# Optimization experiments

Hardware: AMD Instinct MI355X
Metric: run time of the kernel (lower is better)

The kernel has to match this reference:

```python
import jax, jax.numpy as jnp
import numpy as np

D_MODEL = 2048
NHEADS = 16
ROPE_DIM = 64      # config.rope['head_dim']
NOPE_DIM = 128     # config.nope_head_dim
V_DIM = 128        # config.v_head_dim
Q_LORA = 1536      # config.q_lora_rank
KV_LORA = 512      # config.kv_lora_rank
ROPE_BASE = 10000.0
EPS = 1e-6
Q_HEAD = NOPE_DIM + ROPE_DIM   # 192
KV_HEAD = NOPE_DIM + V_DIM     # 256


def rms_norm(x, w):
    return x * jax.lax.rsqrt(jnp.mean(x * x, axis=-1, keepdims=True) + EPS) * w


def apply_rope(x, offset=0):
    # x: (B, H, T, d); standard rotate-half RoPE, positions offset by past length
    d, t = x.shape[-1], x.shape[2]
    inv_freq = 1.0 / (ROPE_BASE ** (jnp.arange(0, d, 2, dtype=jnp.float32) / d))
    pos = jnp.arange(offset, offset + t, dtype=jnp.float32)
    f = pos[:, None] * inv_freq[None, :]          # (T, d/2)
    cos = jnp.concatenate([jnp.cos(f), jnp.cos(f)], -1).astype(x.dtype)
    sin = jnp.concatenate([jnp.sin(f), jnp.sin(f)], -1).astype(x.dtype)
    x1, x2 = jnp.split(x, 2, axis=-1)
    rot = jnp.concatenate([-x2, x1], -1)
    return x * cos + rot * sin


def setup_inputs() -> dict:
    key = jax.random.key(0)
    ks = jax.random.split(key, 8)
    s = 0.02
    return {
        'x': jax.random.normal(ks[0], (2, 2048, D_MODEL), jnp.float32),
        'q_a_w': jax.random.normal(ks[1], (D_MODEL, Q_LORA), jnp.float32) * s,
        'q_a_norm_w': jnp.ones((Q_LORA,), jnp.float32),
        'q_b_w': jax.random.normal(ks[2], (Q_LORA, NHEADS * Q_HEAD), jnp.float32) * s,
        'kv_a_w': jax.random.normal(ks[3], (D_MODEL, KV_LORA + ROPE_DIM), jnp.float32) * s,
        'kv_norm_w': jnp.ones((KV_LORA,), jnp.float32),
        'kv_b_w': jax.random.normal(ks[4], (KV_LORA, NHEADS * KV_HEAD), jnp.float32) * s,
        'o_w': jax.random.normal(ks[5], (NHEADS * V_DIM, D_MODEL), jnp.float32) * s,
    }


def reference(x, q_a_w, q_a_norm_w, q_b_w, kv_a_w, kv_norm_w, kv_b_w, o_w):
    B, T, _ = x.shape
    # Query: LoRA down-proj -> RMSNorm -> up-proj
    q = rms_norm(x @ q_a_w, q_a_norm_w) @ q_b_w            # (B,T,H*Q_HEAD)
    q = q.reshape(B, T, NHEADS, Q_HEAD).transpose(0, 2, 1, 3)
    q_nope, q_rope = q[..., :NOPE_DIM], q[..., NOPE_DIM:]
    # KV: joint compressed projection, split into latent + shared rope key
    kv = x @ kv_a_w                                         # (B,T,KV_LORA+ROPE_DIM)
    kv_c, k_rope = kv[..., :KV_LORA], kv[..., KV_LORA:]
    k_rope = k_rope[:, None, :, :]                          # (B,1,T,ROPE_DIM) - MQA rope key
    kvb = rms_norm(kv_c, kv_norm_w) @ kv_b_w                # (B,T,H*KV_HEAD)
    kvb = kvb.reshape(B, T, NHEADS, KV_HEAD).transpose(0, 2, 1, 3)
    k_nope, v = kvb[..., :NOPE_DIM], kvb[..., NOPE_DIM:]
    # Decoupled RoPE (prefill: offset 0)
    q_rope = apply_rope(q_rope)
    k_rope = apply_rope(k_rope)
    qs = jnp.concatenate([q_nope, q_rope], -1)              # (B,H,T,Q_HEAD)
    ks = jnp.concatenate([k_nope, jnp.broadcast_to(k_rope, (B, NHEADS, T, ROPE_DIM))], -1)
    # SDPA with causal mask, scale = 1/sqrt(q_head_dim)
    scale = 1.0 / np.sqrt(Q_HEAD).astype(np.float32)
    scores = jnp.einsum('bhqd,bhkd->bhqk', qs, ks) * scale
    mask = jnp.tril(jnp.ones((T, T), bool))
    scores = jnp.where(mask[None, None], scores, jnp.finfo(scores.dtype).min)
    attn = jax.nn.softmax(scores, axis=-1)
    out = jnp.einsum('bhqk,bhkd->bhqd', attn, v)            # (B,H,T,V_DIM)
    out = out.transpose(0, 2, 1, 3).reshape(B, T, NHEADS * V_DIM)
    return out @ o_w                                        # (B,T,d_model)
```

## Files before the change

### kernel.cpp

```cpp
#include <hip/hip_runtime.h>
#include <hip/hip_bf16.h>
#include <math.h>

#define NHEADS 16
#define SEQ 2048
#define BATCH 2
#define NTOK (BATCH * SEQ)
#define EPSF 1e-6f

typedef short bf16x8 __attribute__((ext_vector_type(8)));
typedef float f32x4 __attribute__((ext_vector_type(4)));

__device__ __forceinline__ unsigned short f2bf(float v) {
    __hip_bfloat16 h = __float2bfloat16(v);
    return *reinterpret_cast<unsigned short*>(&h);
}
__device__ __forceinline__ float bf2f(unsigned short u) {
    __hip_bfloat16 h = *reinterpret_cast<__hip_bfloat16*>(&u);
    return __bfloat162float(h);
}
__device__ __forceinline__ void g2l16(const void* g, void* l) {
    __builtin_amdgcn_global_load_lds(
        (const __attribute__((address_space(1))) void*)g,
        (__attribute__((address_space(3))) void*)l, 16, 0, 0);
}

#define ROPE_L2 0.4152410118609203f

__global__ __launch_bounds__(256) void cvt_bf16(
    const float* __restrict__ in, unsigned short* __restrict__ out)
{
    const int i = blockIdx.x * 256 + threadIdx.x;
    float4 a = ((const float4*)in)[i * 2];
    float4 b = ((const float4*)in)[i * 2 + 1];
    unsigned short o[8] = {f2bf(a.x), f2bf(a.y), f2bf(a.z), f2bf(a.w),
                           f2bf(b.x), f2bf(b.y), f2bf(b.z), f2bf(b.w)};
    *(bf16x8*)(out + (size_t)i * 8) = *(bf16x8*)o;
}

struct WSeg { const float* src; unsigned short* dst; int Nw, K, nx, off; };
struct WSegs { WSeg s[5]; };

__global__ __launch_bounds__(256) void prep_weights(WSegs segs)
{
    __shared__ float T[32][33];
    const int bid = blockIdx.x;
    int si = 0;
#pragma unroll
    for (int i = 1; i < 5; ++i) si += (bid >= segs.s[i].off) ? 1 : 0;
    const WSeg sg = segs.s[si];
    const int local = bid - sg.off;
    const int bx = local % sg.nx, by = local / sg.nx;
    const int n0 = bx * 32, k0 = by * 32;
    const int tid = threadIdx.x;
    const int r = tid >> 3, c4 = (tid & 7) * 4;
    const bool valid = (n0 < sg.Nw);
    if (valid) {
        float4 v = *(const float4*)(sg.src + (size_t)(k0 + r) * sg.Nw + n0 + c4);
        T[r][c4 + 0] = v.x; T[r][c4 + 1] = v.y; T[r][c4 + 2] = v.z; T[r][c4 + 3] = v.w;
    }
    __syncthreads();
    unsigned short o[4];
#pragma unroll
    for (int j = 0; j < 4; ++j) o[j] = valid ? f2bf(T[c4 + j][r]) : (unsigned short)0;
    *(ulong1*)(sg.dst + (size_t)(n0 + r) * sg.K + k0 + c4) = *(ulong1*)o;
}

template <int OUT_BF16>
__global__ __launch_bounds__(256) void gemm_bt(
    const unsigned short* __restrict__ A,
    const unsigned short* __restrict__ Bt,
    void* __restrict__ Cv,
    int K, int N)
{
    __shared__ __align__(16) unsigned short As[128 * 32];
    __shared__ __align__(16) unsigned short Bs[128 * 32];
    const int tid = threadIdx.x;
    const int lane = tid & 63, wid = tid >> 6;
    const int l16 = lane & 15, lq = lane >> 4;
    const int wr = wid >> 1, wc = wid & 1;
    const int bm = blockIdx.y * 128, bn = blockIdx.x * 128;

    f32x4 acc[4][4];
#pragma unroll
    for (int m = 0; m < 4; ++m)
#pragma unroll
        for (int n = 0; n < 4; ++n) acc[m][n] = (f32x4){0.f, 0.f, 0.f, 0.f};

    for (int k0 = 0; k0 < K; k0 += 32) {
        __syncthreads();
#pragma unroll
        for (int t = 0; t < 2; ++t) {
            const int chunk = t * 256 + tid;
            const int row = chunk >> 2, koff = (chunk & 3) << 3;
            g2l16(A  + (size_t)(bm + row) * K + k0 + koff, (char*)As + chunk * 16);
            g2l16(Bt + (size_t)(bn + row) * K + k0 + koff, (char*)Bs + chunk * 16);
        }
        __syncthreads();

        bf16x8 af[4], bfr[4];
#pragma unroll
        for (int m = 0; m < 4; ++m)
            af[m] = *(const bf16x8*)(As + (wr * 64 + m * 16 + l16) * 32 + lq * 8);
#pragma unroll
        for (int n = 0; n < 4; ++n)
            bfr[n] = *(const bf16x8*)(Bs + (wc * 64 + n * 16 + l16) * 32 + lq * 8);
#pragma unroll
        for (int m = 0; m < 4; ++m)
#pragma unroll
            for (int n = 0; n < 4; ++n)
                acc[m][n] = __builtin_amdgcn_mfma_f32_16x16x32_bf16(af[m], bfr[n], acc[m][n], 0, 0, 0);
    }

#pragma unroll
    for (int m = 0; m < 4; ++m)
#pragma unroll
        for (int n = 0; n < 4; ++n)
#pragma unroll
            for (int reg = 0; reg < 4; ++reg) {
                const int row = bm + wr * 64 + m * 16 + lq * 4 + reg;
                const int col = bn + wc * 64 + n * 16 + l16;
                if (OUT_BF16) ((unsigned short*)Cv)[(size_t)row * N + col] = f2bf(acc[m][n][reg]);
                else          ((float*)Cv)[(size_t)row * N + col] = acc[m][n][reg];
            }
}

__global__ __launch_bounds__(256) void rmsnorm_bf(
    const float* __restrict__ in, const float* __restrict__ w,
    unsigned short* __restrict__ out, int in_stride, int cols)
{
    const int row = blockIdx.x;
    const float* p = in + (size_t)row * in_stride;
    float ss = 0.f;
    for (int c = threadIdx.x; c < cols; c += 256) { float v = p[c]; ss += v * v; }
#pragma unroll
    for (int off = 32; off > 0; off >>= 1) ss += __shfl_down(ss, off, 64);
    __shared__ float wsum[4];
    __shared__ float s_scale;
    const int wave = threadIdx.x >> 6;
    if ((threadIdx.x & 63) == 0) wsum[wave] = ss;
    __syncthreads();
    if (threadIdx.x == 0) {
        float t = wsum[0] + wsum[1] + wsum[2] + wsum[3];
        s_scale = rsqrtf(t / (float)cols + EPSF);
    }
    __syncthreads();
    const float sc = s_scale;
    for (int c = threadIdx.x; c < cols; c += 256)
        out[(size_t)row * cols + c] = f2bf(p[c] * sc * w[c]);
}

__global__ __launch_bounds__(256) void rmsnorm_kv_rope(
    const float* __restrict__ in, const float* __restrict__ w,
    unsigned short* __restrict__ kv_out, unsigned short* __restrict__ krope_out)
{
    const int row = blockIdx.x;
    const float* p = in + (size_t)row * 2176;
    const int tid = threadIdx.x;
    float v0 = p[tid], v1 = p[tid + 256];
    float ss = v0 * v0 + v1 * v1;
#pragma unroll
    for (int off = 32; off > 0; off >>= 1) ss += __shfl_down(ss, off, 64);
    __shared__ float wsum[4];
    __shared__ float s_scale;
    const int wave = tid >> 6;
    if ((tid & 63) == 0) wsum[wave] = ss;
    __syncthreads();
    if (tid == 0) {
        float t = wsum[0] + wsum[1] + wsum[2] + wsum[3];
        s_scale = rsqrtf(t / 512.0f + EPSF);
    }
    __syncthreads();
    const float sc = s_scale;
    kv_out[(size_t)row * 512 + tid]       = f2bf(v0 * sc * w[tid]);
    kv_out[(size_t)row * 512 + tid + 256] = f2bf(v1 * sc * w[tid + 256]);
    if (tid < 64) {
        const int s = row & (SEQ - 1);
        const int j = tid, jj = j & 31;
        float inv = exp2f(-ROPE_L2 * (float)jj);
        float f = (float)s * inv;
        float sn, cs;
        sincosf(f, &sn, &cs);
        const float* kb = p + 512;
        float v = (j < 32) ? (kb[j] * cs - kb[j + 32] * sn)
                           : (kb[j] * cs + kb[j - 32] * sn);
        krope_out[(size_t)row * 64 + j] = f2bf(v);
    }
}

__global__ __launch_bounds__(256) void pack_vt(
    const unsigned short* __restrict__ kvb, unsigned short* __restrict__ vt_bf)
{
    __shared__ __align__(16) unsigned short T[64][136];
    const int st = blockIdx.x, h = blockIdx.y, b = blockIdx.z;
    const int tid = threadIdx.x;
#pragma unroll
    for (int t = 0; t < 4; ++t) {
        int i = tid + t * 256;
        int r = i >> 4, c8 = i & 15;
        bf16x8 v = *(const bf16x8*)(kvb + (size_t)(b * SEQ + st * 64 + r) * 4096 + h * 256 + 128 + c8 * 8);
        *(bf16x8*)&T[r][c8 * 8] = v;
    }
    __syncthreads();
    const int d = tid >> 1, sh = (tid & 1) * 32;
    unsigned short tmp[32];
#pragma unroll
    for (int k = 0; k < 32; ++k) tmp[k] = T[sh + k][d];
    unsigned short* dst = vt_bf + ((size_t)(b * NHEADS + h) * 128 + d) * SEQ + st * 64 + sh;
#pragma unroll
    for (int c = 0; c < 4; ++c) *(bf16x8*)(dst + c * 8) = *(bf16x8*)&tmp[c * 8];
}

#define KPD 200
#define VPD 72
#define PPD 72

__global__ __launch_bounds__(256) void flash_mfma(
    const unsigned short* __restrict__ qbuf,
    const unsigned short* __restrict__ kvb,
    const unsigned short* __restrict__ krope,
    const unsigned short* __restrict__ vt,
    unsigned short* __restrict__ ctx)
{
    __shared__ __align__(16) unsigned short Ks[64][KPD];
    __shared__ __align__(16) unsigned short Vs[128][VPD];
    __shared__ __align__(16) unsigned short Ps[4][16][PPD];
    const int id = blockIdx.x;
    const int xcd = id & 7, sl = id >> 3;
    const int grp = sl >> 4, pair = sl & 15;
    const int hb = xcd + 8 * grp;
    const int h = hb & 15, b = hb >> 4;
    const int tid = threadIdx.x;
    const int wid = tid >> 6, lane = tid & 63;
    const int l16 = lane & 15, lq = lane >> 4;

    const size_t headV = (size_t)(b * NHEADS + h) * 128 * SEQ;
    const float scale = 0.07216878364870323f;

    float cs8[8], sn8[8];
    const int vrow = tid >> 1, vg = tid & 1;

    bf16x8 kn[4], kr[2], vv[4];

#define FLASH_LOAD(KT)                                                          \
    {                                                                           \
        const int tk0_ = b * SEQ + (KT) * 64;                                   \
        _Pragma("unroll")                                                       \
        for (int t = 0; t < 4; ++t) {                                           \
            int i_ = tid + t * 256, r_ = i_ >> 4, c8_ = i_ & 15;                \
            kn[t] = *(const bf16x8*)(kvb + (size_t)(tk0_ + r_) * 4096 + h * 256 + c8_ * 8); \
        }                                                                       \
        _Pragma("unroll")                                                       \
        for (int t = 0; t < 2; ++t) {                                           \
            int i_ = tid + t * 256, r_ = i_ >> 3, c8_ = i_ & 7;                 \
            kr[t] = *(const bf16x8*)(krope + (size_t)(tk0_ + r_) * 64 + c8_ * 8); \
        }                                                                       \
        const unsigned short* vsrc_ = vt + headV + (size_t)vrow * SEQ + (KT) * 64 + vg * 8; \
        _Pragma("unroll")                                                       \
        for (int j = 0; j < 4; ++j) vv[j] = *(const bf16x8*)(vsrc_ + j * 16);   \
    }

#pragma unroll
    for (int pass = 0; pass < 2; ++pass) {
        const int qt = pass ? (31 - pair) : pair;
        const int srow = qt * 64 + wid * 16 + l16;

        bf16x8 qf[6];
        {
            const unsigned short* qp = qbuf + (size_t)(b * SEQ + srow) * 3072 + h * 192 + lq * 8;
            bf16x8 raw[6];
#pragma unroll
            for (int kk = 0; kk < 6; ++kk) raw[kk] = *(const bf16x8*)(qp + kk * 32);
#pragma unroll
            for (int jj = 0; jj < 8; ++jj) {
                float inv = exp2f(-ROPE_L2 * (float)(lq * 8 + jj));
                sincosf((float)srow * inv, &sn8[jj], &cs8[jj]);
            }
#pragma unroll
            for (int kk = 0; kk < 4; ++kk) {
                unsigned short o[8];
#pragma unroll
                for (int e = 0; e < 8; ++e) o[e] = f2bf(bf2f(((unsigned short*)&raw[kk])[e]) * scale);
                qf[kk] = *(bf16x8*)o;
            }
            unsigned short o4[8], o5[8];
#pragma unroll
            for (int e = 0; e < 8; ++e) {
                float x1 = bf2f(((unsigned short*)&raw[4])[e]);
                float x2 = bf2f(((unsigned short*)&raw[5])[e]);
                o4[e] = f2bf((x1 * cs8[e] - x2 * sn8[e]) * scale);
                o5[e] = f2bf((x2 * cs8[e] + x1 * sn8[e]) * scale);
            }
            qf[4] = *(bf16x8*)o4;
            qf[5] = *(bf16x8*)o5;
        }

        f32x4 o[8];
#pragma unroll
        for (int f = 0; f < 8; ++f) o[f] = (f32x4){0.f, 0.f, 0.f, 0.f};
        float m[4] = {-1e30f, -1e30f, -1e30f, -1e30f};
        float lsum[4] = {0.f, 0.f, 0.f, 0.f};

        const int nkt = qt + 1;
        FLASH_LOAD(0);
        for (int kt = 0; kt < nkt; ++kt) {
            __syncthreads();
#pragma unroll
            for (int t = 0; t < 4; ++t) {
                int i = tid + t * 256, r = i >> 4, c8 = i & 15;
                *(bf16x8*)&Ks[r][c8 * 8] = kn[t];
            }
#pragma unroll
            for (int t = 0; t < 2; ++t) {
                int i = tid + t * 256, r = i >> 3, c8 = i & 7;
                *(bf16x8*)&Ks[r][128 + c8 * 8] = kr[t];
            }
#pragma unroll
            for (int j = 0; j < 4; ++j)
                *(bf16x8*)&Vs[vrow][(vg + j * 2) * 8] = vv[j];
            __syncthreads();
            if (kt + 1 < nkt) FLASH_LOAD(kt + 1);

            f32x4 s[4];
#pragma unroll
            for (int f = 0; f < 4; ++f) s[f] = (f32x4){0.f, 0.f, 0.f, 0.f};
            __builtin_amdgcn_s_setprio(1);
#pragma unroll
            for (int f = 0; f < 4; ++f) {
#pragma unroll
                for (int kk = 0; kk < 6; ++kk) {
                    bf16x8 bfr = *(const bf16x8*)&Ks[f * 16 + l16][kk * 32 + lq * 8];
                    s[f] = __builtin_amdgcn_mfma_f32_16x16x32_bf16(qf[kk], bfr, s[f], 0, 0, 0);
                }
            }
            __builtin_amdgcn_s_setprio(0);

            const int qabs = qt * 64 + wid * 16 + lq * 4;
            const bool diag = (kt == qt);
#pragma unroll
            for (int reg = 0; reg < 4; ++reg) {
                float a0 = s[0][reg], a1 = s[1][reg], a2 = s[2][reg], a3 = s[3][reg];
                if (diag) {
                    int q = qabs + reg;
                    int k0 = kt * 64 + l16;
                    if (k0      > q) a0 = -1e30f;
                    if (k0 + 16 > q) a1 = -1e30f;
                    if (k0 + 32 > q) a2 = -1e30f;
                    if (k0 + 48 > q) a3 = -1e30f;
                }
                float rmax = fmaxf(fmaxf(a0, a1), fmaxf(a2, a3));
                rmax = fmaxf(rmax, __shfl_xor(rmax, 1, 64));
                rmax = fmaxf(rmax, __shfl_xor(rmax, 2, 64));
                rmax = fmaxf(rmax, __shfl_xor(rmax, 4, 64));
                rmax = fmaxf(rmax, __shfl_xor(rmax, 8, 64));
                float mnew = fmaxf(m[reg], rmax);
                float sc = __expf(m[reg] - mnew);
                m[reg] = mnew;
                float p0 = __expf(a0 - mnew), p1 = __expf(a1 - mnew);
                float p2 = __expf(a2 - mnew), p3 = __expf(a3 - mnew);
                float rs = p0 + p1 + p2 + p3;
                rs += __shfl_xor(rs, 1, 64);
                rs += __shfl_xor(rs, 2, 64);
                rs += __shfl_xor(rs, 4, 64);
                rs += __shfl_xor(rs, 8, 64);
                lsum[reg] = lsum[reg] * sc + rs;
#pragma unroll
                for (int f = 0; f < 8; ++f) o[f][reg] *= sc;
                Ps[wid][lq * 4 + reg][ 0 + l16] = f2bf(p0);
                Ps[wid][lq * 4 + reg][16 + l16] = f2bf(p1);
                Ps[wid][lq * 4 + reg][32 + l16] = f2bf(p2);
                Ps[wid][lq * 4 + reg][48 + l16] = f2bf(p3);
            }

            bf16x8 pa0 = *(const bf16x8*)&Ps[wid][l16][lq * 8];
            bf16x8 pa1 = *(const bf16x8*)&Ps[wid][l16][32 + lq * 8];
            __builtin_amdgcn_s_setprio(1);
#pragma unroll
            for (int f = 0; f < 8; ++f) {
                bf16x8 b0 = *(const bf16x8*)&Vs[f * 16 + l16][lq * 8];
                bf16x8 b1 = *(const bf16x8*)&Vs[f * 16 + l16][32 + lq * 8];
                o[f] = __builtin_amdgcn_mfma_f32_16x16x32_bf16(pa0, b0, o[f], 0, 0, 0);
                o[f] = __builtin_amdgcn_mfma_f32_16x16x32_bf16(pa1, b1, o[f], 0, 0, 0);
            }
            __builtin_amdgcn_s_setprio(0);
        }

#pragma unroll
        for (int reg = 0; reg < 4; ++reg) {
            float inv = 1.0f / lsum[reg];
            unsigned short* dst = ctx + (size_t)(b * SEQ + qt * 64 + wid * 16 + lq * 4 + reg) * 2048 + h * 128 + l16;
#pragma unroll
            for (int f = 0; f < 8; ++f) dst[f * 16] = f2bf(o[f][reg] * inv);
        }
    }
#undef FLASH_LOAD
}

extern "C" void kernel_launch(void* const* d_in, const int* in_sizes, int n_in,
                              void* d_out, int out_size, void* d_ws, size_t ws_size,
                              hipStream_t stream) {
    const float* x          = (const float*)d_in[0];
    const float* q_a_w      = (const float*)d_in[1];
    const float* q_a_norm_w = (const float*)d_in[2];
    const float* q_b_w      = (const float*)d_in[3];
    const float* kv_a_w     = (const float*)d_in[4];
    const float* kv_norm_w  = (const float*)d_in[5];
    const float* kv_b_w     = (const float*)d_in[6];
    const float* o_w        = (const float*)d_in[7];
    float* out = (float*)d_out;

    char* ws = (char*)d_ws;
    float*          qkv_cat  = (float*)(ws + 0);
    unsigned short* ctx_bf   = (unsigned short*)(ws + 0);
    unsigned short* qbuf_bf  = (unsigned short*)(ws + 35651584);
    unsigned short* vt_bf    = (unsigned short*)(ws + 60817408);
    unsigned short* kvb_bf   = (unsigned short*)(ws + 77594624);
    unsigned short* x_bf     = (unsigned short*)(ws + 111149056);
    unsigned short* q_a_bf   = (unsigned short*)(ws + 111149056);
    unsigned short* kv_c_bf  = (unsigned short*)(ws + 127926272);
    unsigned short* krope_bf = (unsigned short*)(ws + 132120576);
    unsigned short* wcat     = (unsigned short*)(ws + 132644864);
    unsigned short* wkva_t   = wcat + (size_t)1536 * 2048;
    unsigned short* wqb_t    = (unsigned short*)(ws + 141557760);
    unsigned short* wkvb_t   = (unsigned short*)(ws + 150994944);
    unsigned short* wo_t     = (unsigned short*)(ws + 155189248);

    dim3 blk(256);

    cvt_bf16<<<4096, blk, 0, stream>>>(x, x_bf);
    WSegs segs;
    segs.s[0] = { q_a_w,  wcat,   1536, 2048,  48,     0 };
    segs.s[1] = { q_b_w,  wqb_t,  3072, 1536,  96,  3072 };
    segs.s[2] = { kv_a_w, wkva_t,  576, 2048,  20,  7680 };
    segs.s[3] = { kv_b_w, wkvb_t, 4096,  512, 128,  8960 };
    segs.s[4] = { o_w,    wo_t,   2048, 2048,  64, 11008 };
    prep_weights<<<15104, blk, 0, stream>>>(segs);

    gemm_bt<0><<<dim3(17, 32), blk, 0, stream>>>(x_bf, wcat, qkv_cat, 2048, 2176);

    rmsnorm_bf<<<NTOK, blk, 0, stream>>>(qkv_cat, q_a_norm_w, q_a_bf, 2176, 1536);
    rmsnorm_kv_rope<<<NTOK, blk, 0, stream>>>(qkv_cat + 1536, kv_norm_w, kv_c_bf, krope_bf);

    gemm_bt<1><<<dim3(24, 32), blk, 0, stream>>>(q_a_bf, wqb_t, qbuf_bf, 1536, 3072);
    gemm_bt<1><<<dim3(32, 32), blk, 0, stream>>>(kv_c_bf, wkvb_t, kvb_bf, 512, 4096);

    pack_vt<<<dim3(SEQ / 64, NHEADS, BATCH), blk, 0, stream>>>(kvb_bf, vt_bf);

    flash_mfma<<<dim3(512), blk, 0, stream>>>(qbuf_bf, kvb_bf, krope_bf, vt_bf, ctx_bf);

    gemm_bt<0><<<dim3(16, 32), blk, 0, stream>>>(ctx_bf, wo_t, out, 2048, 2048);
}
```

Measured before the change: 386.5 us.

## Use lazy softmax rescale and MFMA row-sum, drop register prefetch

```diff
diff --git a/kernel.cpp b/kernel.cpp
--- a/kernel.cpp
+++ b/kernel.cpp
@@ -214,6 +214,7 @@
 #define KPD 200
 #define VPD 72
 #define PPD 72
+#define RESCALE_THR 8.0f
 
 __global__ __launch_bounds__(256) void flash_mfma(
     const unsigned short* __restrict__ qbuf,
@@ -223,7 +224,7 @@
     unsigned short* __restrict__ ctx)
 {
     __shared__ __align__(16) unsigned short Ks[64][KPD];
-    __shared__ __align__(16) unsigned short Vs[128][VPD];
+    __shared__ __align__(16) unsigned short Vs[144][VPD];
     __shared__ __align__(16) unsigned short Ps[4][16][PPD];
     const int id = blockIdx.x;
     const int xcd = id & 7, sl = id >> 3;
@@ -240,24 +241,11 @@
     float cs8[8], sn8[8];
     const int vrow = tid >> 1, vg = tid & 1;
 
-    bf16x8 kn[4], kr[2], vv[4];
-
-#define FLASH_LOAD(KT)                                                          \
-    {                                                                           \
-        const int tk0_ = b * SEQ + (KT) * 64;                                   \
-        _Pragma("unroll")                                                       \
-        for (int t = 0; t < 4; ++t) {                                           \
-            int i_ = tid + t * 256, r_ = i_ >> 4, c8_ = i_ & 15;                \
-            kn[t] = *(const bf16x8*)(kvb + (size_t)(tk0_ + r_) * 4096 + h * 256 + c8_ * 8); \
-        }                                                                       \
-        _Pragma("unroll")                                                       \
-        for (int t = 0; t < 2; ++t) {                                           \
-            int i_ = tid + t * 256, r_ = i_ >> 3, c8_ = i_ & 7;                 \
-            kr[t] = *(const bf16x8*)(krope + (size_t)(tk0_ + r_) * 64 + c8_ * 8); \
-        }                                                                       \
-        const unsigned short* vsrc_ = vt + headV + (size_t)vrow * SEQ + (KT) * 64 + vg * 8; \
-        _Pragma("unroll")                                                       \
-        for (int j = 0; j < 4; ++j) vv[j] = *(const bf16x8*)(vsrc_ + j * 16);   \
+    {
+        int r = 128 + (tid >> 4);
+        int c = (tid & 15) * 4;
+        unsigned short v = (tid >> 4) == 0 ? (unsigned short)0x3F80 : (unsigned short)0;
+        Vs[r][c] = v; Vs[r][c + 1] = v; Vs[r][c + 2] = v; Vs[r][c + 3] = v;
     }
 
 #pragma unroll
@@ -298,28 +286,34 @@
         f32x4 o[8];
 #pragma unroll
         for (int f = 0; f < 8; ++f) o[f] = (f32x4){0.f, 0.f, 0.f, 0.f};
+        f32x4 oS = (f32x4){0.f, 0.f, 0.f, 0.f};
         float m[4] = {-1e30f, -1e30f, -1e30f, -1e30f};
-        float lsum[4] = {0.f, 0.f, 0.f, 0.f};
 
         const int nkt = qt + 1;
-        FLASH_LOAD(0);
         for (int kt = 0; kt < nkt; ++kt) {
             __syncthreads();
-#pragma unroll
-            for (int t = 0; t < 4; ++t) {
-                int i = tid + t * 256, r = i >> 4, c8 = i & 15;
-                *(bf16x8*)&Ks[r][c8 * 8] = kn[t];
-            }
-#pragma unroll
-            for (int t = 0; t < 2; ++t) {
-                int i = tid + t * 256, r = i >> 3, c8 = i & 7;
-                *(bf16x8*)&Ks[r][128 + c8 * 8] = kr[t];
-            }
-#pragma unroll
-            for (int j = 0; j < 4; ++j)
-                *(bf16x8*)&Vs[vrow][(vg + j * 2) * 8] = vv[j];
+            {
+                const int tk0 = b * SEQ + kt * 64;
+#pragma unroll
+                for (int t = 0; t < 4; ++t) {
+                    int i = tid + t * 256;
+                    int r = i >> 4, c8 = i & 15;
+                    *(bf16x8*)&Ks[r][c8 * 8] =
+                        *(const bf16x8*)(kvb + (size_t)(tk0 + r) * 4096 + h * 256 + c8 * 8);
+                }
+#pragma unroll
+                for (int t = 0; t < 2; ++t) {
+                    int i = tid + t * 256;
+                    int r = i >> 3, c8 = i & 7;
+                    *(bf16x8*)&Ks[r][128 + c8 * 8] =
+                        *(const bf16x8*)(krope + (size_t)(tk0 + r) * 64 + c8 * 8);
+                }
+                const unsigned short* vsrc = vt + headV + (size_t)vrow * SEQ + kt * 64 + vg * 8;
+#pragma unroll
+                for (int j = 0; j < 4; ++j)
+                    *(bf16x8*)&Vs[vrow][(vg + j * 2) * 8] = *(const bf16x8*)(vsrc + j * 16);
+            }
             __syncthreads();
-            if (kt + 1 < nkt) FLASH_LOAD(kt + 1);
 
             f32x4 s[4];
 #pragma unroll
@@ -337,39 +331,43 @@
 
             const int qabs = qt * 64 + wid * 16 + lq * 4;
             const bool diag = (kt == qt);
+            float rmax4[4];
 #pragma unroll
             for (int reg = 0; reg < 4; ++reg) {
-                float a0 = s[0][reg], a1 = s[1][reg], a2 = s[2][reg], a3 = s[3][reg];
                 if (diag) {
                     int q = qabs + reg;
                     int k0 = kt * 64 + l16;
-                    if (k0      > q) a0 = -1e30f;
-                    if (k0 + 16 > q) a1 = -1e30f;
-                    if (k0 + 32 > q) a2 = -1e30f;
-                    if (k0 + 48 > q) a3 = -1e30f;
+                    if (k0      > q) s[0][reg] = -1e30f;
+                    if (k0 + 16 > q) s[1][reg] = -1e30f;
+                    if (k0 + 32 > q) s[2][reg] = -1e30f;
+                    if (k0 + 48 > q) s[3][reg] = -1e30f;
                 }
-                float rmax = fmaxf(fmaxf(a0, a1), fmaxf(a2, a3));
+                float rmax = fmaxf(fmaxf(s[0][reg], s[1][reg]), fmaxf(s[2][reg], s[3][reg]));
                 rmax = fmaxf(rmax, __shfl_xor(rmax, 1, 64));
                 rmax = fmaxf(rmax, __shfl_xor(rmax, 2, 64));
                 rmax = fmaxf(rmax, __shfl_xor(rmax, 4, 64));
                 rmax = fmaxf(rmax, __shfl_xor(rmax, 8, 64));
-                float mnew = fmaxf(m[reg], rmax);
-                float sc = __expf(m[reg] - mnew);
-                m[reg] = mnew;
-                float p0 = __expf(a0 - mnew), p1 = __expf(a1 - mnew);
-                float p2 = __expf(a2 - mnew), p3 = __expf(a3 - mnew);
-                float rs = p0 + p1 + p2 + p3;
-                rs += __shfl_xor(rs, 1, 64);
-                rs += __shfl_xor(rs, 2, 64);
-                rs += __shfl_xor(rs, 4, 64);
-                rs += __shfl_xor(rs, 8, 64);
-                lsum[reg] = lsum[reg] * sc + rs;
-#pragma unroll
-                for (int f = 0; f < 8; ++f) o[f][reg] *= sc;
-                Ps[wid][lq * 4 + reg][ 0 + l16] = f2bf(p0);
-                Ps[wid][lq * 4 + reg][16 + l16] = f2bf(p1);
-                Ps[wid][lq * 4 + reg][32 + l16] = f2bf(p2);
-                Ps[wid][lq * 4 + reg][48 + l16] = f2bf(p3);
+                rmax4[reg] = rmax;
+            }
+            float dmx = fmaxf(fmaxf(rmax4[0] - m[0], rmax4[1] - m[1]),
+                              fmaxf(rmax4[2] - m[2], rmax4[3] - m[3]));
+            if (!__all(dmx <= RESCALE_THR)) {
+#pragma unroll
+                for (int reg = 0; reg < 4; ++reg) {
+                    float mnew = fmaxf(m[reg], rmax4[reg]);
+                    float al = __expf(m[reg] - mnew);
+                    m[reg] = mnew;
+#pragma unroll
+                    for (int f = 0; f < 8; ++f) o[f][reg] *= al;
+                    oS[reg] *= al;
+                }
+            }
+#pragma unroll
+            for (int reg = 0; reg < 4; ++reg) {
+                Ps[wid][lq * 4 + reg][ 0 + l16] = f2bf(__expf(s[0][reg] - m[reg]));
+                Ps[wid][lq * 4 + reg][16 + l16] = f2bf(__expf(s[1][reg] - m[reg]));
+                Ps[wid][lq * 4 + reg][32 + l16] = f2bf(__expf(s[2][reg] - m[reg]));
+                Ps[wid][lq * 4 + reg][48 + l16] = f2bf(__expf(s[3][reg] - m[reg]));
             }
 
             bf16x8 pa0 = *(const bf16x8*)&Ps[wid][l16][lq * 8];
@@ -382,18 +380,24 @@
                 o[f] = __builtin_amdgcn_mfma_f32_16x16x32_bf16(pa0, b0, o[f], 0, 0, 0);
                 o[f] = __builtin_amdgcn_mfma_f32_16x16x32_bf16(pa1, b1, o[f], 0, 0, 0);
             }
+            {
+                bf16x8 s0 = *(const bf16x8*)&Vs[128 + l16][lq * 8];
+                bf16x8 s1 = *(const bf16x8*)&Vs[128 + l16][32 + lq * 8];
+                oS = __builtin_amdgcn_mfma_f32_16x16x32_bf16(pa0, s0, oS, 0, 0, 0);
+                oS = __builtin_amdgcn_mfma_f32_16x16x32_bf16(pa1, s1, oS, 0, 0, 0);
+            }
             __builtin_amdgcn_s_setprio(0);
         }
 
 #pragma unroll
         for (int reg = 0; reg < 4; ++reg) {
-            float inv = 1.0f / lsum[reg];
+            float ls = __shfl(oS[reg], lane & 48, 64);
+            float inv = 1.0f / ls;
             unsigned short* dst = ctx + (size_t)(b * SEQ + qt * 64 + wid * 16 + lq * 4 + reg) * 2048 + h * 128 + l16;
 #pragma unroll
             for (int f = 0; f < 8; ++f) dst[f * 16] = f2bf(o[f][reg] * inv);
         }
     }
-#undef FLASH_LOAD
 }
 
 extern "C" void kernel_launch(void* const* d_in, const int* in_sizes, int n_in,
```

Result: faster. 367.6 us (-4.9%).
